# Kernel tuning notes

Measured on AMD Instinct MI355X. Metric: run time of the kernel, lower is better.

## Reference

```python
import jax, jax.numpy as jnp
import numpy as np

B, S, D, H = 4, 2048, 512, 16
HD = D // H          # head_dim = 32
ROPE_DIM = HD        # rope_pct = 1.0
NEG = -1e30


def apply_rope(x):
    # x: [B, H, S, HD]; rotate first ROPE_DIM dims, half-split (NeoX) convention
    half = ROPE_DIM // 2
    pos = jnp.arange(S, dtype=jnp.float32)
    inv_freq = 1.0 / (10000.0 ** (jnp.arange(0, ROPE_DIM, 2, dtype=jnp.float32) / ROPE_DIM))
    ang = pos[:, None] * inv_freq[None, :]          # [S, half]
    cos, sin = jnp.cos(ang), jnp.sin(ang)           # broadcast over B,H
    x1 = x[..., :half]
    x2 = x[..., half:ROPE_DIM]
    r1 = x1 * cos - x2 * sin
    r2 = x2 * cos + x1 * sin
    rest = x[..., ROPE_DIM:]
    return jnp.concatenate([r1, r2, rest], axis=-1)


def setup_inputs() -> dict:
    key = jax.random.key(0)
    ks = jax.random.split(key, 7)
    x = jax.random.normal(ks[0], (B, S, D), dtype=jnp.float32)
    # causal mask: True = block (j > i)
    attn_mask = jnp.triu(jnp.ones((S, S), dtype=bool), k=1)
    # padding mask: True = PAD; random lengths in [S//2, S]
    lengths = jax.random.randint(ks[1], (B,), S // 2, S + 1)
    key_padding_mask = jnp.arange(S)[None, :] >= lengths[:, None]
    scale = D ** -0.5
    Wq = jax.random.normal(ks[2], (D, D), dtype=jnp.float32) * scale
    Wk = jax.random.normal(ks[3], (D, D), dtype=jnp.float32) * scale
    Wv = jax.random.normal(ks[4], (D, D), dtype=jnp.float32) * scale
    Wo = jax.random.normal(ks[5], (D, D), dtype=jnp.float32) * scale
    return {"x": x, "attn_mask": attn_mask, "key_padding_mask": key_padding_mask,
            "Wq": Wq, "Wk": Wk, "Wv": Wv, "Wo": Wo}


def reference(x, attn_mask, key_padding_mask, Wq, Wk, Wv, Wo):
    scale = HD ** -0.5
    # nn.Linear: y = x @ W.T
    q = (x @ Wq.T).reshape(B, S, H, HD).transpose(0, 2, 1, 3)  # [B,H,S,HD]
    k = (x @ Wk.T).reshape(B, S, H, HD).transpose(0, 2, 1, 3)
    v = (x @ Wv.T).reshape(B, S, H, HD).transpose(0, 2, 1, 3)
    q = apply_rope(q)
    k = apply_rope(k)
    scores = jnp.einsum('bhid,bhjd->bhij', q, k) * scale       # [B,H,S,S]
    scores = jnp.where(key_padding_mask[:, None, None, :], NEG, scores)
    scores = jnp.where(attn_mask[None, None, :, :], NEG, scores)
    probs = jax.nn.softmax(scores.astype(jnp.float32), axis=-1)
    probs = jnp.nan_to_num(probs, nan=0.0)
    ctx = jnp.einsum('bhij,bhjd->bhid', probs, v)              # [B,H,S,HD]
    ctx = ctx.transpose(0, 2, 1, 3).reshape(B, S, D)
    ctx = jnp.where(key_padding_mask[:, :, None], 0.0, ctx)
    return ctx @ Wo.T
```

## Files before the change

### kernel.cpp

```cpp
#include <hip/hip_runtime.h>
#include <hip/hip_bf16.h>

#define B_ 4
#define S_ 2048
#define D_ 512
#define H_ 16
#define HD_ 32

typedef __bf16 bf16;
typedef __bf16 bf16x4 __attribute__((ext_vector_type(4)));
typedef __bf16 bf16x8 __attribute__((ext_vector_type(8)));
typedef float f32x4 __attribute__((ext_vector_type(4)));

__device__ __forceinline__ f32x4 mfma16(bf16x8 a, bf16x8 b, f32x4 c) {
  return __builtin_amdgcn_mfma_f32_16x16x32_bf16(a, b, c, 0, 0, 0);
}

__device__ __forceinline__ void gload16(const bf16* g, bf16* l) {
  __builtin_amdgcn_global_load_lds(
      (const __attribute__((address_space(1))) void*)g,
      (__attribute__((address_space(3))) void*)l, 16, 0, 0);
}

__device__ __forceinline__ bf16x8 cvt8(const float* __restrict__ p) {
  const f32x4* v = (const f32x4*)p;
  f32x4 a = v[0], b = v[1];
  bf16x8 r;
  r[0] = (bf16)a[0]; r[1] = (bf16)a[1]; r[2] = (bf16)a[2]; r[3] = (bf16)a[3];
  r[4] = (bf16)b[0]; r[5] = (bf16)b[1]; r[6] = (bf16)b[2]; r[7] = (bf16)b[3];
  return r;
}

__global__ __launch_bounds__(256) void prep_kernel(
    const float* __restrict__ x, const float* __restrict__ wq,
    const float* __restrict__ wk, const float* __restrict__ wv,
    const float* __restrict__ wo, const unsigned char* __restrict__ am,
    const unsigned char* __restrict__ kpm, bf16* __restrict__ xb,
    bf16* __restrict__ dq, bf16* __restrict__ dk, bf16* __restrict__ dv,
    bf16* __restrict__ dwo, int* __restrict__ lengths_out,
    float* __restrict__ costab, float* __restrict__ sintab) {
  int bid = blockIdx.x;
  if (bid < 2048) {
    size_t i = (size_t)bid * 256 + threadIdx.x;
    *(bf16x8*)(xb + i * 8) = cvt8(x + i * 8);
  } else if (bid < 2560) {
    int wb = bid - 2048;
    int mat = wb >> 7;
    size_t i = (size_t)(wb & 127) * 256 + threadIdx.x;
    const float* s = (mat == 0) ? wq : (mat == 1) ? wk : (mat == 2) ? wv : wo;
    bf16* d = (mat == 0) ? dq : (mat == 1) ? dk : (mat == 2) ? dv : dwo;
    *(bf16x8*)(d + i * 8) = cvt8(s + i * 8);
  } else if (bid == 2560) {
    int b = threadIdx.x >> 6, lane = threadIdx.x & 63;
    int esize;
    if (am[1] == 1) esize = 1;
    else if (am[2] == 0x80 && am[3] == 0x3F) esize = 2;
    else if (am[3] == 0x3C) esize = 2;
    else if (am[4] == 1) esize = 4;
    else if (am[6] == 0x80 && am[7] == 0x3F) esize = 4;
    else if (am[8] == 1) esize = 8;
    else esize = 1;
    int cnt = 0;
    for (int i = lane; i < S_; i += 64) {
      size_t off = ((size_t)b * S_ + i) * (size_t)esize;
      unsigned char nz = 0;
      for (int e = 0; e < esize; ++e) nz |= kpm[off + e];
      cnt += (nz == 0) ? 1 : 0;
    }
    for (int off = 1; off < 64; off <<= 1) cnt += __shfl_xor(cnt, off);
    if (lane == 0) lengths_out[b] = cnt;
  } else {
    int ti = (bid - 2561) * 256 + threadIdx.x;
    int s = ti >> 4, cc = ti & 15;
    float invf = powf(10000.0f, -(float)cc * (1.0f / 16.0f));
    float ang = (float)s * invf;
    costab[ti] = cosf(ang);
    sintab[ti] = sinf(ang);
  }
}

#define LDT 136
__global__ __launch_bounds__(256) void qkv_rope_kernel(
    const bf16* __restrict__ x, const bf16* __restrict__ Wq,
    const bf16* __restrict__ Wk, const bf16* __restrict__ Wv,
    const float* __restrict__ costab, const float* __restrict__ sintab,
    bf16* __restrict__ q_ws, bf16* __restrict__ k_ws, bf16* __restrict__ vt_ws) {
  __shared__ __align__(16) bf16 smem[17408];
#define AS(b) (smem + (b) * 4096)
#define BS(b) (smem + 8192 + (b) * 4096)
#define CT smem

  int bid = blockIdx.x;
  int brow = bid / 12, bc = bid % 12;
  int mat = bc >> 2;
  const bf16* W = (mat == 0) ? Wq : (mat == 1) ? Wk : Wv;
  int row0 = brow * 128;
  int col0 = (bc & 3) * 128;

  int tid = threadIdx.x;
  int w = tid >> 6, l = tid & 63;
  int wr = w >> 1, wc = w & 1;
  int g = l >> 4, c = l & 15;
  int lrow = l >> 2;
  int lcol = (l & 3) * 8;

  f32x4 acc[4][4];
  f32x4 zero = {0.f, 0.f, 0.f, 0.f};
#pragma unroll
  for (int m = 0; m < 4; ++m)
#pragma unroll
    for (int n = 0; n < 4; ++n) acc[m][n] = zero;

#pragma unroll
  for (int j = 0; j < 2; ++j) {
    int chunk = w * 2 + j;
    int grow = chunk * 16 + lrow;
    gload16(x + (size_t)(row0 + grow) * 512 + lcol, AS(0) + chunk * 512);
    gload16(W + (size_t)(col0 + grow) * 512 + lcol, BS(0) + chunk * 512);
  }
  __syncthreads();
  int cur = 0;

#pragma unroll 1
  for (int k0 = 0; k0 < 512; k0 += 32) {
    bool more = (k0 < 480);
    if (more) {
#pragma unroll
      for (int j = 0; j < 2; ++j) {
        int chunk = w * 2 + j;
        int grow = chunk * 16 + lrow;
        gload16(x + (size_t)(row0 + grow) * 512 + k0 + 32 + lcol,
                AS(cur ^ 1) + chunk * 512);
        gload16(W + (size_t)(col0 + grow) * 512 + k0 + 32 + lcol,
                BS(cur ^ 1) + chunk * 512);
      }
    }
    bf16x8 af[4], bfr[4];
#pragma unroll
    for (int m = 0; m < 4; ++m)
      af[m] = *(const bf16x8*)(AS(cur) + (wr * 64 + m * 16 + c) * 32 + g * 8);
#pragma unroll
    for (int n = 0; n < 4; ++n)
      bfr[n] = *(const bf16x8*)(BS(cur) + (wc * 64 + n * 16 + c) * 32 + g * 8);
#pragma unroll
    for (int m = 0; m < 4; ++m)
#pragma unroll
      for (int n = 0; n < 4; ++n) acc[m][n] = mfma16(af[m], bfr[n], acc[m][n]);
    if (more) {
      __syncthreads();
      cur ^= 1;
    }
  }

  if (mat < 2) {
    bf16* dst = (mat == 0) ? q_ws : k_ws;
#pragma unroll
    for (int m = 0; m < 4; ++m) {
      int rbase = row0 + wr * 64 + m * 16 + g * 4;
#pragma unroll
      for (int r = 0; r < 4; ++r) {
        int grow = rbase + r;
        int bb = grow >> 11, s = grow & (S_ - 1);
        float cs = costab[s * 16 + c];
        float sn = sintab[s * 16 + c];
#pragma unroll
        for (int np = 0; np < 2; ++np) {
          int n = np * 2;
          int obase = col0 + wc * 64 + n * 16;
          int h = obase >> 5;
          float a0 = acc[m][n][r], a1 = acc[m][n + 1][r];
          size_t base = (((size_t)bb * H_ + h) * S_ + s) * HD_;
          dst[base + c] = (bf16)(a0 * cs - a1 * sn);
          dst[base + c + 16] = (bf16)(a1 * cs + a0 * sn);
        }
      }
    }
  } else {
    __syncthreads();
#pragma unroll
    for (int m = 0; m < 4; ++m) {
#pragma unroll
      for (int n = 0; n < 4; ++n) {
        int o = wc * 64 + n * 16 + c;
        int sb = wr * 64 + m * 16 + g * 4;
        bf16x4 q4;
        q4[0] = (bf16)acc[m][n][0]; q4[1] = (bf16)acc[m][n][1];
        q4[2] = (bf16)acc[m][n][2]; q4[3] = (bf16)acc[m][n][3];
        *(bf16x4*)(&CT[o * LDT + sb]) = q4;
      }
    }
    __syncthreads();
    int o_l = tid >> 1, sh = (tid & 1) * 64;
    int o = col0 + o_l;
    int h = o >> 5, hd = o & 31;
    int bb2 = row0 >> 11, sr = row0 & (S_ - 1);
    size_t dst = (((size_t)bb2 * H_ + h) * HD_ + hd) * S_ + sr + sh;
#pragma unroll
    for (int j = 0; j < 8; ++j)
      *(bf16x8*)(vt_ws + dst + j * 8) =
          *(const bf16x8*)(&CT[o_l * LDT + sh + j * 8]);
  }
#undef AS
#undef BS
#undef CT
}

__global__ __launch_bounds__(256) void attn_kernel(
    const bf16* __restrict__ q_ws, const bf16* __restrict__ k_ws,
    const bf16* __restrict__ vt_ws, const int* __restrict__ lengths,
    bf16* __restrict__ ctx_ws) {
  __shared__ __align__(16) bf16 Ks[2][2048];
  __shared__ __align__(16) bf16 Vts[2][2048];
  __shared__ __align__(16) bf16 Ps[4][1024];

  int p = blockIdx.x;
  int bh = blockIdx.y;
  int bb = bh >> 4, h = bh & 15;
  int tid = threadIdx.x, w = tid >> 6, l = tid & 63, g = l >> 4, c = l & 15;
  const size_t bh_base = ((size_t)bb * H_ + h) * (size_t)S_ * HD_;
  const float escale = 0.17677669529663687f * 1.4426950408889634f;
  int len = lengths[bb];
  int rowrel = w * 16 + c;

  int srowK = w * 16 + (l & 15), skgK = l >> 4;
  int srowV = w * 8 + (l & 7), ssgV = l >> 3;
  int slotK8 = (skgK * 16 + (srowK & 15) + ((srowK >> 4) << 6)) * 8;
  int slotV8 =
      ((ssgV & 3) * 16 + (srowV & 15) + (((ssgV >> 2) + ((srowV >> 4) << 1)) << 6)) * 8;

  bf16 one = (bf16)1.0f;
  bf16x8 onesf;
#pragma unroll
  for (int i = 0; i < 8; ++i) onesf[i] = one;

#pragma unroll 1
  for (int phase = 0; phase < 2; ++phase) {
    int qt = phase ? (31 - p) : p;
    int q0 = qt * 64 + w * 16;

    bf16x8 qf = *(const bf16x8*)(q_ws + bh_base + (size_t)(q0 + c) * HD_ + g * 8);

    f32x4 zero = {0.f, 0.f, 0.f, 0.f};
    f32x4 ctxa[2];
    ctxa[0] = zero; ctxa[1] = zero;
    f32x4 lsum = zero;

    const bf16* kptr = k_ws + bh_base + (size_t)srowK * HD_ + skgK * 8;
    const bf16* vptr = vt_ws + bh_base + (size_t)srowV * S_ + ssgV * 8;

    bf16x8 regK = *(const bf16x8*)kptr;
    bf16x8 regV = *(const bf16x8*)vptr;
    kptr += 64 * HD_;
    vptr += 64;
    __syncthreads();
    *(bf16x8*)(&Ks[0][slotK8]) = regK;
    *(bf16x8*)(&Vts[0][slotV8]) = regV;
    __syncthreads();
    int cur = 0;

#pragma unroll 1
    for (int kt = 0; kt <= qt; ++kt) {
      bool hasNext = (kt < qt);
      if (hasNext) {
        regK = *(const bf16x8*)kptr;
        regV = *(const bf16x8*)vptr;
        kptr += 64 * HD_;
        vptr += 64;
      }
      const bf16* KsC = Ks[cur];
      const bf16* VtsC = Vts[cur];

      f32x4 sacc[4];
#pragma unroll
      for (int n = 0; n < 4; ++n) {
        bf16x8 kf = *(const bf16x8*)(&KsC[(l + (n << 6)) * 8]);
        sacc[n] = mfma16(kf, qf, zero);
      }

      float sv[4][4];
      if (kt != qt) {
#pragma unroll
        for (int n = 0; n < 4; ++n)
#pragma unroll
          for (int r = 0; r < 4; ++r)
            sv[n][r] = __builtin_amdgcn_exp2f(sacc[n][r] * escale);
      } else {
#pragma unroll
        for (int n = 0; n < 4; ++n) {
          int jr = n * 16 + g * 4;
#pragma unroll
          for (int r = 0; r < 4; ++r) {
            float e = __builtin_amdgcn_exp2f(sacc[n][r] * escale);
            sv[n][r] = (jr + r > rowrel) ? 0.f : e;
          }
        }
      }

#pragma unroll
      for (int n = 0; n < 4; ++n) {
        bf16x4 pk;
        pk[0] = (bf16)sv[n][0]; pk[1] = (bf16)sv[n][1];
        pk[2] = (bf16)sv[n][2]; pk[3] = (bf16)sv[n][3];
        int chunk = 2 * n + (g >> 1);
        int off = ((chunk >> 2) << 9) + ((chunk & 3) * 16 + c) * 8 + ((g & 1) << 2);
        *(bf16x4*)(&Ps[w][off]) = pk;
      }

      bf16x8 pf0 = *(const bf16x8*)(&Ps[w][l * 8]);
      bf16x8 pf1 = *(const bf16x8*)(&Ps[w][512 + l * 8]);

      lsum = mfma16(pf0, onesf, lsum);
      lsum = mfma16(pf1, onesf, lsum);

#pragma unroll
      for (int n2 = 0; n2 < 2; ++n2) {
        bf16x8 v0 = *(const bf16x8*)(&VtsC[(l + ((2 * n2) << 6)) * 8]);
        bf16x8 v1 = *(const bf16x8*)(&VtsC[(l + ((1 + 2 * n2) << 6)) * 8]);
        ctxa[n2] = mfma16(pf0, v0, ctxa[n2]);
        ctxa[n2] = mfma16(pf1, v1, ctxa[n2]);
      }

      if (hasNext) {
        *(bf16x8*)(&Ks[cur ^ 1][slotK8]) = regK;
        *(bf16x8*)(&Vts[cur ^ 1][slotV8]) = regV;
        __syncthreads();
        cur ^= 1;
      }
    }

#pragma unroll
    for (int n = 0; n < 2; ++n)
#pragma unroll
      for (int r = 0; r < 4; ++r) {
        int qr = q0 + g * 4 + r;
        float val = ctxa[n][r] / lsum[r];
        if (qr >= len) val = 0.f;
        ctx_ws[(((size_t)bb * S_ + qr) * H_ + h) * HD_ + n * 16 + c] = (bf16)val;
      }
  }
}

__global__ __launch_bounds__(256) void out_proj_kernel(
    const bf16* __restrict__ ctx, const bf16* __restrict__ Wo,
    float* __restrict__ out) {
  __shared__ __align__(16) bf16 As[2][4096];
  __shared__ __align__(16) bf16 Bs[2][4096];

  int bid = blockIdx.x;
  int brow = bid >> 2, bc = bid & 3;
  int row0 = brow * 128, col0 = bc * 128;
  int tid = threadIdx.x;
  int w = tid >> 6, l = tid & 63;
  int wr = w >> 1, wc = w & 1;
  int g = l >> 4, c = l & 15;
  int lrow = l >> 2;
  int lcol = (l & 3) * 8;

  f32x4 acc[4][4];
  f32x4 zero = {0.f, 0.f, 0.f, 0.f};
#pragma unroll
  for (int m = 0; m < 4; ++m)
#pragma unroll
    for (int n = 0; n < 4; ++n) acc[m][n] = zero;

#pragma unroll
  for (int j = 0; j < 2; ++j) {
    int chunk = w * 2 + j;
    int grow = chunk * 16 + lrow;
    gload16(ctx + (size_t)(row0 + grow) * 512 + lcol, As[0] + chunk * 512);
    gload16(Wo + (size_t)(col0 + grow) * 512 + lcol, Bs[0] + chunk * 512);
  }
  __syncthreads();
  int cur = 0;

#pragma unroll 1
  for (int k0 = 0; k0 < 512; k0 += 32) {
    bool more = (k0 < 480);
    if (more) {
#pragma unroll
      for (int j = 0; j < 2; ++j) {
        int chunk = w * 2 + j;
        int grow = chunk * 16 + lrow;
        gload16(ctx + (size_t)(row0 + grow) * 512 + k0 + 32 + lcol,
                As[cur ^ 1] + chunk * 512);
        gload16(Wo + (size_t)(col0 + grow) * 512 + k0 + 32 + lcol,
                Bs[cur ^ 1] + chunk * 512);
      }
    }
    bf16x8 af[4], bfr[4];
#pragma unroll
    for (int m = 0; m < 4; ++m)
      af[m] = *(const bf16x8*)(As[cur] + (wr * 64 + m * 16 + c) * 32 + g * 8);
#pragma unroll
    for (int n = 0; n < 4; ++n)
      bfr[n] = *(const bf16x8*)(Bs[cur] + (wc * 64 + n * 16 + c) * 32 + g * 8);
#pragma unroll
    for (int m = 0; m < 4; ++m)
#pragma unroll
      for (int n = 0; n < 4; ++n) acc[m][n] = mfma16(af[m], bfr[n], acc[m][n]);
    if (more) {
      __syncthreads();
      cur ^= 1;
    }
  }

#pragma unroll
  for (int m = 0; m < 4; ++m) {
    int rbase = row0 + wr * 64 + m * 16 + g * 4;
#pragma unroll
    for (int n = 0; n < 4; ++n) {
      int o = col0 + wc * 64 + n * 16 + c;
#pragma unroll
      for (int r = 0; r < 4; ++r)
        out[(size_t)(rbase + r) * 512 + o] = acc[m][n][r];
    }
  }
}

extern "C" void kernel_launch(void* const* d_in, const int* in_sizes, int n_in,
                              void* d_out, int out_size, void* d_ws,
                              size_t ws_size, hipStream_t stream) {
  const float* x = (const float*)d_in[0];
  const unsigned char* am = (const unsigned char*)d_in[1];
  const unsigned char* kpm = (const unsigned char*)d_in[2];
  const float* Wq = (const float*)d_in[3];
  const float* Wk = (const float*)d_in[4];
  const float* Wv = (const float*)d_in[5];
  const float* Wo = (const float*)d_in[6];
  float* out = (float*)d_out;

  char* ws = (char*)d_ws;
  int* lengths = (int*)ws;
  const size_t QKV_ELEMS = (size_t)B_ * H_ * S_ * HD_;
  const size_t W_ELEMS = (size_t)D_ * D_;
  bf16* xb = (bf16*)(ws + 256);
  bf16* q_ws = xb + QKV_ELEMS;
  bf16* k_ws = q_ws + QKV_ELEMS;
  bf16* vt_ws = k_ws + QKV_ELEMS;
  bf16* wqb = vt_ws + QKV_ELEMS;
  bf16* wkb = wqb + W_ELEMS;
  bf16* wvb = wkb + W_ELEMS;
  bf16* wob = wvb + W_ELEMS;
  float* costab = (float*)(wob + W_ELEMS);
  float* sintab = costab + (size_t)S_ * 16;
  bf16* ctx_ws = xb;

  hipLaunchKernelGGL(prep_kernel, dim3(2689), dim3(256), 0, stream, x, Wq, Wk,
                     Wv, Wo, am, kpm, xb, wqb, wkb, wvb, wob, lengths, costab,
                     sintab);
  hipLaunchKernelGGL(qkv_rope_kernel, dim3(768), dim3(256), 0, stream, xb, wqb,
                     wkb, wvb, costab, sintab, q_ws, k_ws, vt_ws);
  hipLaunchKernelGGL(attn_kernel, dim3(16, 64), dim3(256), 0, stream, q_ws, k_ws,
                     vt_ws, lengths, ctx_ws);
  hipLaunchKernelGGL(out_proj_kernel, dim3(256), dim3(256), 0, stream, ctx_ws,
                     wob, out);
}
```

Before: 122.2 us.

## Load K fragments directly into registers and fold softmax scale into Q

The attention kernel stops staging K tiles through shared memory. Each lane now loads its MFMA K fragments straight from global memory into two ping-ponged register sets, with the loop manually unrolled by two so the buffers alternate. The softmax scale and log2(e) factor are folded into Q during the projection epilogue, which removes a multiply per score in the exp2 step. This cuts LDS traffic and per-element VALU work, at the cost of more registers and less-coalesced global K loads.

```diff
diff --git a/kernel.cpp b/kernel.cpp
--- a/kernel.cpp
+++ b/kernel.cpp
@@ -154,6 +154,8 @@
 
   if (mat < 2) {
     bf16* dst = (mat == 0) ? q_ws : k_ws;
+    const float esc =
+        (mat == 0) ? (0.17677669529663687f * 1.4426950408889634f) : 1.0f;
 #pragma unroll
     for (int m = 0; m < 4; ++m) {
       int rbase = row0 + wr * 64 + m * 16 + g * 4;
@@ -170,8 +172,8 @@
           int h = obase >> 5;
           float a0 = acc[m][n][r], a1 = acc[m][n + 1][r];
           size_t base = (((size_t)bb * H_ + h) * S_ + s) * HD_;
-          dst[base + c] = (bf16)(a0 * cs - a1 * sn);
-          dst[base + c + 16] = (bf16)(a1 * cs + a0 * sn);
+          dst[base + c] = (bf16)((a0 * cs - a1 * sn) * esc);
+          dst[base + c + 16] = (bf16)((a1 * cs + a0 * sn) * esc);
         }
       }
     }
@@ -209,7 +211,6 @@
     const bf16* __restrict__ q_ws, const bf16* __restrict__ k_ws,
     const bf16* __restrict__ vt_ws, const int* __restrict__ lengths,
     bf16* __restrict__ ctx_ws) {
-  __shared__ __align__(16) bf16 Ks[2][2048];
   __shared__ __align__(16) bf16 Vts[2][2048];
   __shared__ __align__(16) bf16 Ps[4][1024];
 
@@ -218,13 +219,10 @@
   int bb = bh >> 4, h = bh & 15;
   int tid = threadIdx.x, w = tid >> 6, l = tid & 63, g = l >> 4, c = l & 15;
   const size_t bh_base = ((size_t)bb * H_ + h) * (size_t)S_ * HD_;
-  const float escale = 0.17677669529663687f * 1.4426950408889634f;
   int len = lengths[bb];
   int rowrel = w * 16 + c;
 
-  int srowK = w * 16 + (l & 15), skgK = l >> 4;
   int srowV = w * 8 + (l & 7), ssgV = l >> 3;
-  int slotK8 = (skgK * 16 + (srowK & 15) + ((srowK >> 4) << 6)) * 8;
   int slotV8 =
       ((ssgV & 3) * 16 + (srowV & 15) + (((ssgV >> 2) + ((srowV >> 4) << 1)) << 6)) * 8;
 
@@ -232,6 +230,8 @@
   bf16x8 onesf;
 #pragma unroll
   for (int i = 0; i < 8; ++i) onesf[i] = one;
+
+  const bf16* kfbase = k_ws + bh_base + (size_t)c * HD_ + g * 8;
 
 #pragma unroll 1
   for (int phase = 0; phase < 2; ++phase) {
@@ -245,52 +245,37 @@
     ctxa[0] = zero; ctxa[1] = zero;
     f32x4 lsum = zero;
 
-    const bf16* kptr = k_ws + bh_base + (size_t)srowK * HD_ + skgK * 8;
+    bf16x8 kA[4], kB[4];
     const bf16* vptr = vt_ws + bh_base + (size_t)srowV * S_ + ssgV * 8;
 
-    bf16x8 regK = *(const bf16x8*)kptr;
+#pragma unroll
+    for (int n = 0; n < 4; ++n)
+      kA[n] = *(const bf16x8*)(kfbase + (size_t)n * 16 * HD_);
     bf16x8 regV = *(const bf16x8*)vptr;
-    kptr += 64 * HD_;
     vptr += 64;
     __syncthreads();
-    *(bf16x8*)(&Ks[0][slotK8]) = regK;
     *(bf16x8*)(&Vts[0][slotV8]) = regV;
     __syncthreads();
-    int cur = 0;
-
-#pragma unroll 1
-    for (int kt = 0; kt <= qt; ++kt) {
-      bool hasNext = (kt < qt);
-      if (hasNext) {
-        regK = *(const bf16x8*)kptr;
-        regV = *(const bf16x8*)vptr;
-        kptr += 64 * HD_;
-        vptr += 64;
-      }
-      const bf16* KsC = Ks[cur];
-      const bf16* VtsC = Vts[cur];
-
+
+    auto body = [&](const bf16x8(&kfr)[4], const bf16* VtsC, int ktcur) {
       f32x4 sacc[4];
 #pragma unroll
-      for (int n = 0; n < 4; ++n) {
-        bf16x8 kf = *(const bf16x8*)(&KsC[(l + (n << 6)) * 8]);
-        sacc[n] = mfma16(kf, qf, zero);
-      }
+      for (int n = 0; n < 4; ++n) sacc[n] = mfma16(kfr[n], qf, zero);
 
       float sv[4][4];
-      if (kt != qt) {
+      if (ktcur != qt) {
 #pragma unroll
         for (int n = 0; n < 4; ++n)
 #pragma unroll
           for (int r = 0; r < 4; ++r)
-            sv[n][r] = __builtin_amdgcn_exp2f(sacc[n][r] * escale);
+            sv[n][r] = __builtin_amdgcn_exp2f(sacc[n][r]);
       } else {
 #pragma unroll
         for (int n = 0; n < 4; ++n) {
           int jr = n * 16 + g * 4;
 #pragma unroll
           for (int r = 0; r < 4; ++r) {
-            float e = __builtin_amdgcn_exp2f(sacc[n][r] * escale);
+            float e = __builtin_amdgcn_exp2f(sacc[n][r]);
             sv[n][r] = (jr + r > rowrel) ? 0.f : e;
           }
         }
@@ -319,13 +304,40 @@
         ctxa[n2] = mfma16(pf0, v0, ctxa[n2]);
         ctxa[n2] = mfma16(pf1, v1, ctxa[n2]);
       }
-
+    };
+
+    int kt = 0;
+#pragma unroll 1
+    while (true) {
+      bool hasNext = (kt < qt);
       if (hasNext) {
-        *(bf16x8*)(&Ks[cur ^ 1][slotK8]) = regK;
-        *(bf16x8*)(&Vts[cur ^ 1][slotV8]) = regV;
-        __syncthreads();
-        cur ^= 1;
-      }
+        const bf16* kb = kfbase + (size_t)(kt + 1) * 64 * HD_;
+#pragma unroll
+        for (int n = 0; n < 4; ++n)
+          kB[n] = *(const bf16x8*)(kb + (size_t)n * 16 * HD_);
+        regV = *(const bf16x8*)vptr;
+        vptr += 64;
+      }
+      body(kA, Vts[0], kt);
+      if (!hasNext) break;
+      *(bf16x8*)(&Vts[1][slotV8]) = regV;
+      __syncthreads();
+      ++kt;
+
+      hasNext = (kt < qt);
+      if (hasNext) {
+        const bf16* kb = kfbase + (size_t)(kt + 1) * 64 * HD_;
+#pragma unroll
+        for (int n = 0; n < 4; ++n)
+          kA[n] = *(const bf16x8*)(kb + (size_t)n * 16 * HD_);
+        regV = *(const bf16x8*)vptr;
+        vptr += 64;
+      }
+      body(kB, Vts[1], kt);
+      if (!hasNext) break;
+      *(bf16x8*)(&Vts[0][slotV8]) = regV;
+      __syncthreads();
+      ++kt;
     }
 
 #pragma unroll
```

Measured after the change: 142.9 us. +17.0%, slower.
